# Optimization experiments

Hardware: AMD Instinct MI355X
Metric: run time of the kernel (lower is better)

## Reference

```python
import jax, jax.numpy as jnp
import numpy as np

B, N, D, T = 4, 512, 128, 1000

def setup_inputs() -> dict:
    key = jax.random.key(0)
    ks = jax.random.split(key, 8)
    s = 0.02  # init scale
    return {
        "adj_noisy": jax.random.randint(ks[0], (B, N, N), 0, 2, dtype=jnp.int32),
        "t": jax.random.randint(ks[1], (B,), 0, T + 1, dtype=jnp.int32),
        "time_embed": jax.random.normal(ks[2], (T + 1, D), dtype=jnp.float32) * s,
        "no_cond_embed": jnp.zeros((D,), dtype=jnp.float32),
        "edge_embed": jax.random.normal(ks[3], (2, D), dtype=jnp.float32) * s,
        "W1": jax.random.normal(ks[4], (3 * D, D), dtype=jnp.float32) * s,
        "b1": jnp.zeros((D,), dtype=jnp.float32),
        "W2": jax.random.normal(ks[5], (D, D), dtype=jnp.float32) * s,
        "b2": jnp.zeros((D,), dtype=jnp.float32),
        "Wc": jax.random.normal(ks[6], (2 * D, 2), dtype=jnp.float32) * s,
        "bc": jnp.zeros((2,), dtype=jnp.float32),
    }


def reference(adj_noisy, t, time_embed, no_cond_embed, edge_embed, W1, b1, W2, b2, Wc, bc):
    d = time_embed.shape[1]
    b, n, _ = adj_noisy.shape
    # time embedding broadcast to [B, N, D]
    t_emb = jnp.broadcast_to(time_embed[t][:, None, :], (b, n, d))
    # encode_noisy_graph: mean over j of edge_embed[adj[b,i,j]]. Since adj in {0,1},
    # mean of gathered rows == (1-p)*E[0] + p*E[1] with p = fraction of ones (exact same math).
    p = adj_noisy.astype(jnp.float32).mean(axis=2)  # [B, N]
    H_noisy = (1.0 - p)[..., None] * edge_embed[0] + p[..., None] * edge_embed[1]
    # uncond path: H_prev = no_cond_embed broadcast
    H_prev = jnp.broadcast_to(no_cond_embed[None, None, :], (b, n, d))
    # fusion MLP on [B, N, 3D]
    x = jnp.concatenate([H_noisy, H_prev, t_emb], axis=-1)
    h = jax.nn.relu(jnp.einsum('bnf,fd->bnd', x, W1) + b1)
    H_fused = jax.nn.relu(jnp.einsum('bnd,de->bne', h, W2) + b2)
    # edge classifier on concat([H_i, H_j]): split Wc so we never materialize [B,N,N,2D].
    li = jnp.einsum('bnd,dc->bnc', H_fused, Wc[:d])  # contribution of H_i
    lj = jnp.einsum('bnd,dc->bnc', H_fused, Wc[d:])  # contribution of H_j
    logits = li[:, :, None, :] + lj[:, None, :, :] + bc  # [B, N, N, 2]
    return logits
```

## Files before the change

### kernel.cpp

```cpp
#include <hip/hip_runtime.h>
#include <hip/hip_bf16.h>

#define DD 128
#define NN 512
#define BB 4

__global__ __launch_bounds__(256) void rows_kernel(
    const int* __restrict__ adj,
    const int* __restrict__ tt,
    const float* __restrict__ time_embed,
    const float* __restrict__ no_cond,
    const float* __restrict__ edge_embed,
    const float* __restrict__ W1,
    const float* __restrict__ b1,
    const float* __restrict__ W2,
    const float* __restrict__ b2,
    const float* __restrict__ Wc,
    const float* __restrict__ bc,
    float* __restrict__ ws_li,
    float* __restrict__ ws_lj)
{
    __shared__ float sP[8 * 8 * DD];
    __shared__ float s_cb[DD];
    __shared__ float s_v1[DD];
    __shared__ float s_p[8];
    __shared__ float s_rc[256];
    __shared__ float s_rv[256];

    const int t = threadIdx.x;
    const int row0 = blockIdx.x * 8;
    const int b = blockIdx.x >> 6;

    {
        const int d = t & 127;
        const int h = t >> 7;
        const float* teb = time_embed + (size_t)tt[b] * DD;
        float c = 0.f, v = 0.f;
        if (h == 0) {
#pragma unroll 4
            for (int k = 0; k < 128; ++k)
                c = fmaf(edge_embed[k], W1[k * DD + d], c);
#pragma unroll 4
            for (int k = 0; k < 64; ++k)
                c = fmaf(no_cond[k], W1[(128 + k) * DD + d], c);
#pragma unroll 4
            for (int k = 64; k < 128; ++k)
                v = fmaf(edge_embed[DD + k] - edge_embed[k], W1[k * DD + d], v);
        } else {
#pragma unroll 4
            for (int k = 64; k < 128; ++k)
                c = fmaf(no_cond[k], W1[(128 + k) * DD + d], c);
#pragma unroll 4
            for (int k = 0; k < 128; ++k)
                c = fmaf(teb[k], W1[(256 + k) * DD + d], c);
#pragma unroll 4
            for (int k = 0; k < 64; ++k)
                v = fmaf(edge_embed[DD + k] - edge_embed[k], W1[k * DD + d], v);
        }
        s_rc[t] = c;
        s_rv[t] = v;
    }

    const int cg = t & 31;
    const int dh = t >> 5;

    {
        const int4* base = (const int4*)(adj + (size_t)(row0 + dh) * NN);
        int s = 0;
#pragma unroll
        for (int k = 0; k < 4; ++k) {
            int4 a = base[cg + 32 * k];
            s += a.x + a.y + a.z + a.w;
        }
#pragma unroll
        for (int off = 16; off; off >>= 1) s += __shfl_xor(s, off, 64);
        if (cg == 0) s_p[dh] = (float)s * (1.0f / (float)NN);
    }
    __syncthreads();

    if (t < DD) {
        s_cb[t] = s_rc[t] + s_rc[t + 128] + b1[t];
        s_v1[t] = s_rv[t] + s_rv[t + 128];
    }
    __syncthreads();

    float p[8];
#pragma unroll
    for (int r = 0; r < 8; ++r) p[r] = s_p[r];

    const int c0 = cg * 4;
    float acc[8][4];
#pragma unroll
    for (int r = 0; r < 8; ++r)
#pragma unroll
        for (int cc = 0; cc < 4; ++cc) acc[r][cc] = 0.f;

    const float4* W2v = (const float4*)W2;
#pragma unroll
    for (int i = 0; i < 16; ++i) {
        const int d = dh * 16 + i;
        float4 w = W2v[(d * DD + c0) >> 2];
        float cbd = s_cb[d];
        float v1d = s_v1[d];
#pragma unroll
        for (int r = 0; r < 8; ++r) {
            float h = fmaxf(fmaf(p[r], v1d, cbd), 0.f);
            acc[r][0] = fmaf(h, w.x, acc[r][0]);
            acc[r][1] = fmaf(h, w.y, acc[r][1]);
            acc[r][2] = fmaf(h, w.z, acc[r][2]);
            acc[r][3] = fmaf(h, w.w, acc[r][3]);
        }
    }
#pragma unroll
    for (int r = 0; r < 8; ++r) {
        float4 v = make_float4(acc[r][0], acc[r][1], acc[r][2], acc[r][3]);
        *(float4*)&sP[(r * 8 + dh) * DD + c0] = v;
    }
    __syncthreads();

    float s0 = 0.f, s1 = 0.f, s2 = 0.f, s3 = 0.f;
#pragma unroll
    for (int k = 0; k < 8; ++k) {
        float4 v = *(const float4*)&sP[(dh * 8 + k) * DD + c0];
        s0 += v.x; s1 += v.y; s2 += v.z; s3 += v.w;
    }
    float4 bb = *(const float4*)&b2[c0];
    float f0 = fmaxf(s0 + bb.x, 0.f);
    float f1 = fmaxf(s1 + bb.y, 0.f);
    float f2 = fmaxf(s2 + bb.z, 0.f);
    float f3 = fmaxf(s3 + bb.w, 0.f);

    const float4* WcV = (const float4*)Wc;
    float4 wa0 = WcV[(c0 * 2) >> 2];
    float4 wa1 = WcV[(c0 * 2 + 4) >> 2];
    float4 wb0 = WcV[((DD + c0) * 2) >> 2];
    float4 wb1 = WcV[((DD + c0) * 2 + 4) >> 2];

    float li0 = f0 * wa0.x + f1 * wa0.z + f2 * wa1.x + f3 * wa1.z;
    float li1 = f0 * wa0.y + f1 * wa0.w + f2 * wa1.y + f3 * wa1.w;
    float lj0 = f0 * wb0.x + f1 * wb0.z + f2 * wb1.x + f3 * wb1.z;
    float lj1 = f0 * wb0.y + f1 * wb0.w + f2 * wb1.y + f3 * wb1.w;

#pragma unroll
    for (int off = 16; off; off >>= 1) {
        li0 += __shfl_xor(li0, off, 64);
        li1 += __shfl_xor(li1, off, 64);
        lj0 += __shfl_xor(lj0, off, 64);
        lj1 += __shfl_xor(lj1, off, 64);
    }
    if (cg == 0) {
        int row = row0 + dh;
        *(float2*)&ws_li[row * 2] = make_float2(li0 + bc[0], li1 + bc[1]);
        *(float2*)&ws_lj[row * 2] = make_float2(lj0, lj1);
    }
}

__global__ __launch_bounds__(256) void write_kernel(
    const float* __restrict__ ws_li,
    const float* __restrict__ ws_lj,
    float* __restrict__ out)
{
    const int blk = blockIdx.x;
    const int t = threadIdx.x;
    const int b = blk >> 8;
    const int i = (blk & 255) * 2 + (t >> 7);
    const int j0 = (t & 127) * 4;

    float2 li = *(const float2*)&ws_li[(b * NN + i) * 2];
    float a0 = li.x;
    float a1 = li.y;

    float4 L0 = *(const float4*)&ws_lj[(b * NN + j0) * 2];
    float4 L1 = *(const float4*)&ws_lj[(b * NN + j0 + 2) * 2];

    float4 o0 = make_float4(a0 + L0.x, a1 + L0.y, a0 + L0.z, a1 + L0.w);
    float4 o1 = make_float4(a0 + L1.x, a1 + L1.y, a0 + L1.z, a1 + L1.w);

    size_t base = (((size_t)(b * NN + i)) * NN + j0) * 2;
    *(float4*)&out[base]     = o0;
    *(float4*)&out[base + 4] = o1;
}

extern "C" void kernel_launch(void* const* d_in, const int* in_sizes, int n_in,
                              void* d_out, int out_size, void* d_ws, size_t ws_size,
                              hipStream_t stream) {
    const int*   adj = (const int*)d_in[0];
    const int*   tt  = (const int*)d_in[1];
    const float* te  = (const float*)d_in[2];
    const float* nc  = (const float*)d_in[3];
    const float* ee  = (const float*)d_in[4];
    const float* W1  = (const float*)d_in[5];
    const float* b1  = (const float*)d_in[6];
    const float* W2  = (const float*)d_in[7];
    const float* b2  = (const float*)d_in[8];
    const float* Wc  = (const float*)d_in[9];
    const float* bc  = (const float*)d_in[10];
    float* out = (float*)d_out;

    float* ws    = (float*)d_ws;
    float* ws_li = ws;
    float* ws_lj = ws + 4096;

    rows_kernel<<<256, 256, 0, stream>>>(adj, tt, te, nc, ee, W1, b1, W2, b2,
                                         Wc, bc, ws_li, ws_lj);
    write_kernel<<<1024, 256, 0, stream>>>(ws_li, ws_lj, out);
}
```

Measured before the change: 97.36 us.

## Fuse row and write kernels into one cooperative kernel with grid syncs

Merges the per-row MLP kernel and the output broadcast kernel into a single cooperative launch. The W1 constant projection, which every block used to recompute, is now split across 20 blocks into workspace partials and shared after a grid sync. A second grid sync separates the li/lj computation from the output writes, which each block then does for its own 8 rows. This removes the redundant per-block W1 matvec and one kernel launch, at the cost of two grid-wide barriers and the overhead of a cooperative launch.

```diff
diff --git a/kernel.cpp b/kernel.cpp
--- a/kernel.cpp
+++ b/kernel.cpp
@@ -1,11 +1,12 @@
 #include <hip/hip_runtime.h>
-#include <hip/hip_bf16.h>
+#include <hip/hip_cooperative_groups.h>
 
 #define DD 128
 #define NN 512
-#define BB 4
-
-__global__ __launch_bounds__(256) void rows_kernel(
+
+namespace cg = cooperative_groups;
+
+__global__ __launch_bounds__(256) void fused_kernel(
     const int* __restrict__ adj,
     const int* __restrict__ tt,
     const float* __restrict__ time_embed,
@@ -17,78 +18,97 @@
     const float* __restrict__ b2,
     const float* __restrict__ Wc,
     const float* __restrict__ bc,
+    float* __restrict__ ws_cbq,
+    float* __restrict__ ws_v1q,
     float* __restrict__ ws_li,
-    float* __restrict__ ws_lj)
+    float* __restrict__ ws_lj,
+    float* __restrict__ out)
 {
+    cg::grid_group grid = cg::this_grid();
+
     __shared__ float sP[8 * 8 * DD];
     __shared__ float s_cb[DD];
     __shared__ float s_v1[DD];
     __shared__ float s_p[8];
-    __shared__ float s_rc[256];
-    __shared__ float s_rv[256];
-
-    const int t = threadIdx.x;
-    const int row0 = blockIdx.x * 8;
-    const int b = blockIdx.x >> 6;
-
-    {
-        const int d = t & 127;
-        const int h = t >> 7;
-        const float* teb = time_embed + (size_t)tt[b] * DD;
-        float c = 0.f, v = 0.f;
-        if (h == 0) {
-#pragma unroll 4
-            for (int k = 0; k < 128; ++k)
-                c = fmaf(edge_embed[k], W1[k * DD + d], c);
-#pragma unroll 4
-            for (int k = 0; k < 64; ++k)
-                c = fmaf(no_cond[k], W1[(128 + k) * DD + d], c);
-#pragma unroll 4
-            for (int k = 64; k < 128; ++k)
-                v = fmaf(edge_embed[DD + k] - edge_embed[k], W1[k * DD + d], v);
-        } else {
-#pragma unroll 4
-            for (int k = 64; k < 128; ++k)
-                c = fmaf(no_cond[k], W1[(128 + k) * DD + d], c);
-#pragma unroll 4
-            for (int k = 0; k < 128; ++k)
-                c = fmaf(teb[k], W1[(256 + k) * DD + d], c);
-#pragma unroll 4
-            for (int k = 0; k < 64; ++k)
-                v = fmaf(edge_embed[DD + k] - edge_embed[k], W1[k * DD + d], v);
-        }
-        s_rc[t] = c;
-        s_rv[t] = v;
-    }
-
-    const int cg = t & 31;
-    const int dh = t >> 5;
+    __shared__ float s_red[256];
+
+    const int t    = threadIdx.x;
+    const int blk  = blockIdx.x;
+    const int row0 = blk * 8;
+    const int b    = blk >> 6;
+    const int lane = t & 31;
+    const int dh   = t >> 5;
 
     {
         const int4* base = (const int4*)(adj + (size_t)(row0 + dh) * NN);
         int s = 0;
 #pragma unroll
         for (int k = 0; k < 4; ++k) {
-            int4 a = base[cg + 32 * k];
+            int4 a = base[lane + 32 * k];
             s += a.x + a.y + a.z + a.w;
         }
 #pragma unroll
         for (int off = 16; off; off >>= 1) s += __shfl_xor(s, off, 64);
-        if (cg == 0) s_p[dh] = (float)s * (1.0f / (float)NN);
+        if (lane == 0) s_p[dh] = (float)s * (1.0f / (float)NN);
+    }
+
+    if (blk < 16) {
+        const int pb = blk >> 2;
+        const int q  = blk & 3;
+        const int d  = t & 127;
+        const int h  = t >> 7;
+        const float* teb = time_embed + (size_t)tt[pb] * DD;
+        const int k0 = q * 96 + h * 48;
+        float c = 0.f;
+#pragma unroll
+        for (int kk = 0; kk < 48; ++kk) {
+            const int k = k0 + kk;
+            float xv = (k < 128) ? edge_embed[k]
+                     : (k < 256) ? no_cond[k - 128]
+                                 : teb[k - 256];
+            c = fmaf(xv, W1[k * DD + d], c);
+        }
+        s_red[t] = c;
+        __syncthreads();
+        if (t < 128)
+            ws_cbq[(q * 4 + pb) * DD + t] = s_red[t] + s_red[t + 128];
+    } else if (blk < 20) {
+        const int q = blk - 16;
+        const int d = t & 127;
+        const int h = t >> 7;
+        const int k0 = q * 32 + h * 16;
+        float c = 0.f;
+#pragma unroll
+        for (int kk = 0; kk < 16; ++kk) {
+            const int k = k0 + kk;
+            c = fmaf(edge_embed[DD + k] - edge_embed[k], W1[k * DD + d], c);
+        }
+        s_red[t] = c;
+        __syncthreads();
+        if (t < 128)
+            ws_v1q[q * DD + t] = s_red[t] + s_red[t + 128];
+    }
+
+    grid.sync();
+
+    if (t < DD) {
+        float c = b1[t];
+        float v = 0.f;
+#pragma unroll
+        for (int q = 0; q < 4; ++q) {
+            c += ws_cbq[(q * 4 + b) * DD + t];
+            v += ws_v1q[q * DD + t];
+        }
+        s_cb[t] = c;
+        s_v1[t] = v;
     }
     __syncthreads();
 
-    if (t < DD) {
-        s_cb[t] = s_rc[t] + s_rc[t + 128] + b1[t];
-        s_v1[t] = s_rv[t] + s_rv[t + 128];
-    }
-    __syncthreads();
-
     float p[8];
 #pragma unroll
     for (int r = 0; r < 8; ++r) p[r] = s_p[r];
 
-    const int c0 = cg * 4;
+    const int c0 = lane * 4;
     float acc[8][4];
 #pragma unroll
     for (int r = 0; r < 8; ++r)
@@ -118,67 +138,60 @@
     }
     __syncthreads();
 
-    float s0 = 0.f, s1 = 0.f, s2 = 0.f, s3 = 0.f;
-#pragma unroll
-    for (int k = 0; k < 8; ++k) {
-        float4 v = *(const float4*)&sP[(dh * 8 + k) * DD + c0];
-        s0 += v.x; s1 += v.y; s2 += v.z; s3 += v.w;
-    }
-    float4 bb = *(const float4*)&b2[c0];
-    float f0 = fmaxf(s0 + bb.x, 0.f);
-    float f1 = fmaxf(s1 + bb.y, 0.f);
-    float f2 = fmaxf(s2 + bb.z, 0.f);
-    float f3 = fmaxf(s3 + bb.w, 0.f);
-
-    const float4* WcV = (const float4*)Wc;
-    float4 wa0 = WcV[(c0 * 2) >> 2];
-    float4 wa1 = WcV[(c0 * 2 + 4) >> 2];
-    float4 wb0 = WcV[((DD + c0) * 2) >> 2];
-    float4 wb1 = WcV[((DD + c0) * 2 + 4) >> 2];
-
-    float li0 = f0 * wa0.x + f1 * wa0.z + f2 * wa1.x + f3 * wa1.z;
-    float li1 = f0 * wa0.y + f1 * wa0.w + f2 * wa1.y + f3 * wa1.w;
-    float lj0 = f0 * wb0.x + f1 * wb0.z + f2 * wb1.x + f3 * wb1.z;
-    float lj1 = f0 * wb0.y + f1 * wb0.w + f2 * wb1.y + f3 * wb1.w;
-
-#pragma unroll
-    for (int off = 16; off; off >>= 1) {
-        li0 += __shfl_xor(li0, off, 64);
-        li1 += __shfl_xor(li1, off, 64);
-        lj0 += __shfl_xor(lj0, off, 64);
-        lj1 += __shfl_xor(lj1, off, 64);
-    }
-    if (cg == 0) {
-        int row = row0 + dh;
-        *(float2*)&ws_li[row * 2] = make_float2(li0 + bc[0], li1 + bc[1]);
-        *(float2*)&ws_lj[row * 2] = make_float2(lj0, lj1);
-    }
-}
-
-__global__ __launch_bounds__(256) void write_kernel(
-    const float* __restrict__ ws_li,
-    const float* __restrict__ ws_lj,
-    float* __restrict__ out)
-{
-    const int blk = blockIdx.x;
-    const int t = threadIdx.x;
-    const int b = blk >> 8;
-    const int i = (blk & 255) * 2 + (t >> 7);
-    const int j0 = (t & 127) * 4;
-
-    float2 li = *(const float2*)&ws_li[(b * NN + i) * 2];
-    float a0 = li.x;
-    float a1 = li.y;
-
-    float4 L0 = *(const float4*)&ws_lj[(b * NN + j0) * 2];
-    float4 L1 = *(const float4*)&ws_lj[(b * NN + j0 + 2) * 2];
-
-    float4 o0 = make_float4(a0 + L0.x, a1 + L0.y, a0 + L0.z, a1 + L0.w);
-    float4 o1 = make_float4(a0 + L1.x, a1 + L1.y, a0 + L1.z, a1 + L1.w);
-
-    size_t base = (((size_t)(b * NN + i)) * NN + j0) * 2;
-    *(float4*)&out[base]     = o0;
-    *(float4*)&out[base + 4] = o1;
+    {
+        float s0 = 0.f, s1 = 0.f, s2 = 0.f, s3 = 0.f;
+#pragma unroll
+        for (int k = 0; k < 8; ++k) {
+            float4 v = *(const float4*)&sP[(dh * 8 + k) * DD + c0];
+            s0 += v.x; s1 += v.y; s2 += v.z; s3 += v.w;
+        }
+        float4 bb = *(const float4*)&b2[c0];
+        float f0 = fmaxf(s0 + bb.x, 0.f);
+        float f1 = fmaxf(s1 + bb.y, 0.f);
+        float f2 = fmaxf(s2 + bb.z, 0.f);
+        float f3 = fmaxf(s3 + bb.w, 0.f);
+
+        const float4* WcV = (const float4*)Wc;
+        float4 wa0 = WcV[(c0 * 2) >> 2];
+        float4 wa1 = WcV[(c0 * 2 + 4) >> 2];
+        float4 wb0 = WcV[((DD + c0) * 2) >> 2];
+        float4 wb1 = WcV[((DD + c0) * 2 + 4) >> 2];
+
+        float li0 = f0 * wa0.x + f1 * wa0.z + f2 * wa1.x + f3 * wa1.z;
+        float li1 = f0 * wa0.y + f1 * wa0.w + f2 * wa1.y + f3 * wa1.w;
+        float lj0 = f0 * wb0.x + f1 * wb0.z + f2 * wb1.x + f3 * wb1.z;
+        float lj1 = f0 * wb0.y + f1 * wb0.w + f2 * wb1.y + f3 * wb1.w;
+
+#pragma unroll
+        for (int off = 16; off; off >>= 1) {
+            li0 += __shfl_xor(li0, off, 64);
+            li1 += __shfl_xor(li1, off, 64);
+            lj0 += __shfl_xor(lj0, off, 64);
+            lj1 += __shfl_xor(lj1, off, 64);
+        }
+        if (lane == 0) {
+            int row = row0 + dh;
+            *(float2*)&ws_li[row * 2] = make_float2(li0 + bc[0], li1 + bc[1]);
+            *(float2*)&ws_lj[row * 2] = make_float2(lj0, lj1);
+        }
+    }
+
+    grid.sync();
+
+    {
+        const float4* ljv = (const float4*)(ws_lj + (size_t)b * NN * 2);
+        const int r   = t >> 5;
+        const int row = row0 + r;
+        float2 li = *(const float2*)&ws_li[row * 2];
+        const float a0 = li.x, a1 = li.y;
+        float4* orow = (float4*)(out + (size_t)row * NN * 2);
+#pragma unroll
+        for (int k = 0; k < 8; ++k) {
+            const int q = lane + 32 * k;
+            float4 L = ljv[q];
+            orow[q] = make_float4(a0 + L.x, a1 + L.y, a0 + L.z, a1 + L.w);
+        }
+    }
 }
 
 extern "C" void kernel_launch(void* const* d_in, const int* in_sizes, int n_in,
@@ -197,11 +210,17 @@
     const float* bc  = (const float*)d_in[10];
     float* out = (float*)d_out;
 
-    float* ws    = (float*)d_ws;
-    float* ws_li = ws;
-    float* ws_lj = ws + 4096;
-
-    rows_kernel<<<256, 256, 0, stream>>>(adj, tt, te, nc, ee, W1, b1, W2, b2,
-                                         Wc, bc, ws_li, ws_lj);
-    write_kernel<<<1024, 256, 0, stream>>>(ws_li, ws_lj, out);
+    float* ws     = (float*)d_ws;
+    float* ws_cbq = ws;
+    float* ws_v1q = ws + 2048;
+    float* ws_li  = ws + 2560;
+    float* ws_lj  = ws + 6656;
+
+    void* args[] = { (void*)&adj, (void*)&tt, (void*)&te, (void*)&nc,
+                     (void*)&ee, (void*)&W1, (void*)&b1, (void*)&W2,
+                     (void*)&b2, (void*)&Wc, (void*)&bc,
+                     (void*)&ws_cbq, (void*)&ws_v1q, (void*)&ws_li,
+                     (void*)&ws_lj, (void*)&out };
+    hipLaunchCooperativeKernel((const void*)fused_kernel,
+                               dim3(256), dim3(256), args, 0, stream);
 }
```

New measurement: 148.1 us. 52.1% more time.
